# Optimization experiments

Measured on AMD Instinct MI355X. Metric: run time of the kernel, lower is better.

The kernel has to match this reference:

```python
import jax, jax.numpy as jnp
import numpy as np

B, N, DIM = 4, 8192, 1024
HEADS, DIM_HEAD = 16, 64


def setup_inputs() -> dict:
    key = jax.random.key(0)
    ks = jax.random.split(key, 6)
    s = 1.0 / np.sqrt(DIM_HEAD)
    so = 1.0 / np.sqrt(HEADS * DIM_HEAD)
    return {
        "x": jax.random.normal(ks[0], (B, N, DIM), dtype=jnp.float32),
        "Wq": jax.random.uniform(ks[1], (DIM_HEAD, DIM_HEAD), jnp.float32, -s, s),
        "Wk": jax.random.uniform(ks[2], (DIM_HEAD, DIM_HEAD), jnp.float32, -s, s),
        "Wv": jax.random.uniform(ks[3], (DIM_HEAD, DIM_HEAD), jnp.float32, -s, s),
        "Wo": jax.random.uniform(ks[4], (DIM, HEADS * DIM_HEAD), jnp.float32, -so, so),
        "bo": jax.random.uniform(ks[5], (DIM,), jnp.float32, -so, so),
    }


def reference(x, Wq, Wk, Wv, Wo, bo):
    Bs, Ns, Cs = x.shape
    # [B, H, N, Dh]
    xh = x.reshape(Bs, Ns, HEADS, DIM_HEAD).transpose(0, 2, 1, 3)
    # torch Linear: y = x @ W.T
    q = jnp.einsum('bhnd,ed->bhne', xh, Wq)
    k = jnp.einsum('bhnd,ed->bhne', xh, Wk)
    v = jnp.einsum('bhnd,ed->bhne', xh, Wv)
    # k^T v: [B, H, Dh, Dh], normalized by N (dropout is identity, p=0)
    dots = jnp.einsum('bhnd,bhne->bhde', k, v) / float(Ns)
    res = jnp.einsum('bhnd,bhde->bhne', q, dots)
    # b h n d -> b n (h d)
    res = res.transpose(0, 2, 1, 3).reshape(Bs, Ns, HEADS * DIM_HEAD)
    return res @ Wo.T + bo
```

## Files before the change

kernel.cpp:

```cpp
#include <hip/hip_runtime.h>

#define DIMC 1024
#define NSEQ 8192
#define DH 64

typedef __attribute__((ext_vector_type(8))) short short8;
typedef __attribute__((ext_vector_type(4))) float f32x4;

__device__ __forceinline__ short f2bf(float f) {
  union { float f; unsigned u; } v; v.f = f;
  unsigned r = v.u + 0x7FFFu + ((v.u >> 16) & 1u);
  return (short)(r >> 16);
}

__device__ __forceinline__ unsigned pack_bf2(float a, float b) {
  union { float f; unsigned u; } va, vb;
  va.f = a; vb.f = b;
  unsigned ua = va.u + 0x8000u;
  unsigned ub = vb.u + 0x8000u;
  return (ua >> 16) | (ub & 0xFFFF0000u);
}

__device__ __forceinline__ void gload_lds16(const void* g, void* l) {
  __builtin_amdgcn_global_load_lds(
      (const __attribute__((address_space(1))) void*)g,
      (__attribute__((address_space(3))) void*)l, 16, 0, 0);
}

__global__ __launch_bounds__(64) void gram_kernel(const float* __restrict__ x,
                                                  float* __restrict__ Gpart,
                                                  short* __restrict__ xbf) {
  int chunk = blockIdx.x, bh = blockIdx.y;
  int b = bh >> 4, h = bh & 15;
  int t = threadIdx.x;
  __shared__ __align__(16) float rows[16 * 64];
  const float* xb = x + ((size_t)b * NSEQ) * DIMC + h * DH;
  short* xo = xbf ? xbf + ((size_t)b * NSEQ) * DIMC + h * DH : (short*)0;
  int d0 = (t >> 3) * 8, e0 = (t & 7) * 8;
  float acc[8][8] = {};
  float4 v[4];
#pragma unroll
  for (int i = 0; i < 4; i++) {
    int f4 = i * 64 + t;
    v[i] = *(const float4*)(xb + (size_t)(chunk * 256 + (f4 >> 4)) * DIMC + (f4 & 15) * 4);
  }
  for (int it = 0; it < 16; it++) {
    __syncthreads();
#pragma unroll
    for (int i = 0; i < 4; i++) ((float4*)rows)[i * 64 + t] = v[i];
    __syncthreads();
    if (xo) {
#pragma unroll
      for (int i = 0; i < 4; i++) {
        int f4 = i * 64 + t;
        int row = chunk * 256 + it * 16 + (f4 >> 4), col = (f4 & 15) * 4;
        uint2 pw = {pack_bf2(v[i].x, v[i].y), pack_bf2(v[i].z, v[i].w)};
        *(uint2*)(xo + (size_t)row * DIMC + col) = pw;
      }
    }
    if (it < 15) {
      int nbase = chunk * 256 + (it + 1) * 16;
#pragma unroll
      for (int i = 0; i < 4; i++) {
        int f4 = i * 64 + t;
        v[i] = *(const float4*)(xb + (size_t)(nbase + (f4 >> 4)) * DIMC + (f4 & 15) * 4);
      }
    }
#pragma unroll
    for (int r = 0; r < 16; r++) {
      float xd[8], xe[8];
      *(float4*)&xd[0] = *(const float4*)&rows[r * 64 + d0];
      *(float4*)&xd[4] = *(const float4*)&rows[r * 64 + d0 + 4];
      *(float4*)&xe[0] = *(const float4*)&rows[r * 64 + e0];
      *(float4*)&xe[4] = *(const float4*)&rows[r * 64 + e0 + 4];
#pragma unroll
      for (int i = 0; i < 8; i++)
#pragma unroll
        for (int j = 0; j < 8; j++) acc[i][j] = fmaf(xd[i], xe[j], acc[i][j]);
    }
  }
  float* gp = Gpart + (size_t)chunk * (64 * 4096) + (size_t)bh * 4096;
#pragma unroll
  for (int i = 0; i < 8; i++)
#pragma unroll
    for (int j = 0; j < 8; j++) gp[(d0 + i) * 64 + e0 + j] = acc[i][j];
}

__global__ void reduce_g(const float* __restrict__ Gpart, float* __restrict__ G) {
  int i = blockIdx.x * 256 + threadIdx.x;
  float s = 0.f;
#pragma unroll
  for (int p = 0; p < 32; p++) s += Gpart[(size_t)p * (64 * 4096) + i];
  G[i] = s;
}

__global__ __launch_bounds__(256) void combine_kernel(
    const float* __restrict__ G, const float* __restrict__ Wq,
    const float* __restrict__ Wk, const float* __restrict__ Wv,
    const float* __restrict__ Wo, short* __restrict__ WbigT) {
  int bh = blockIdx.x, qt = blockIdx.y;
  int b = bh >> 4, h = bh & 15;
  int t = threadIdx.x;
  __shared__ __align__(16) float sG[4096];
  __shared__ __align__(16) float sW[4096];
  __shared__ __align__(16) float sA[4096];
  __shared__ __align__(16) float sM[4096];

  for (int i = t; i < 4096; i += 256) sG[i] = G[(size_t)bh * 4096 + i];
  for (int i = t; i < 4096; i += 256) sW[i] = Wk[i];
  __syncthreads();

  int d0 = (t >> 4) * 4, e0 = (t & 15) * 4;
  {
    float a[4][4] = {};
    for (int fg = 0; fg < 16; fg++) {
      float wk[4][4], g4[4][4];
#pragma unroll
      for (int i = 0; i < 4; i++) *(float4*)wk[i] = *(const float4*)&sW[(d0 + i) * 64 + fg * 4];
#pragma unroll
      for (int ff = 0; ff < 4; ff++) *(float4*)g4[ff] = *(const float4*)&sG[(fg * 4 + ff) * 64 + e0];
#pragma unroll
      for (int i = 0; i < 4; i++)
#pragma unroll
        for (int ff = 0; ff < 4; ff++)
#pragma unroll
          for (int j = 0; j < 4; j++) a[i][j] = fmaf(wk[i][ff], g4[ff][j], a[i][j]);
    }
#pragma unroll
    for (int i = 0; i < 4; i++)
#pragma unroll
      for (int j = 0; j < 4; j++) sA[(d0 + i) * 64 + e0 + j] = a[i][j];
  }
  __syncthreads();
  for (int i = t; i < 4096; i += 256) sW[i] = Wv[i];
  __syncthreads();
  {
    float a[4][4] = {};
    for (int fgi = 0; fgi < 16; fgi++) {
      int fg = (fgi + (t & 15)) & 15;
      float t1[4][4], wv[4][4];
#pragma unroll
      for (int i = 0; i < 4; i++) *(float4*)t1[i] = *(const float4*)&sA[(d0 + i) * 64 + fg * 4];
#pragma unroll
      for (int j = 0; j < 4; j++) *(float4*)wv[j] = *(const float4*)&sW[(e0 + j) * 64 + fg * 4];
#pragma unroll
      for (int i = 0; i < 4; i++)
#pragma unroll
        for (int j = 0; j < 4; j++)
#pragma unroll
          for (int ff = 0; ff < 4; ff++) a[i][j] = fmaf(t1[i][ff], wv[j][ff], a[i][j]);
    }
    __syncthreads();
#pragma unroll
    for (int i = 0; i < 4; i++)
#pragma unroll
      for (int j = 0; j < 4; j++) sG[(d0 + i) * 64 + e0 + j] = a[i][j];
  }
  __syncthreads();
  for (int i = t; i < 4096; i += 256) sW[i] = Wq[i];
  __syncthreads();
  {
    float a[4][4] = {};
    for (int f = 0; f < 64; f++) {
      float wq[4], t2[4];
      *(float4*)wq = *(const float4*)&sW[f * 64 + d0];
      *(float4*)t2 = *(const float4*)&sG[f * 64 + e0];
#pragma unroll
      for (int i = 0; i < 4; i++)
#pragma unroll
        for (int j = 0; j < 4; j++) a[i][j] = fmaf(wq[i], t2[j], a[i][j]);
    }
#pragma unroll
    for (int i = 0; i < 4; i++)
#pragma unroll
      for (int j = 0; j < 4; j++) sM[(d0 + i) * 64 + e0 + j] = a[i][j] * (1.0f / 8192.0f);
  }
  __syncthreads();
  int dd0 = (t & 15) * 4, cl0 = (t >> 4) * 4;
  for (int cc = qt * 2; cc < qt * 2 + 2; cc++) {
    int c0 = cc * 64;
    for (int i = t; i < 4096; i += 256)
      sW[i] = Wo[(size_t)(c0 + (i >> 6)) * DIMC + h * DH + (i & 63)];
    __syncthreads();
    float a[4][4] = {};
    for (int egi = 0; egi < 16; egi++) {
      int eg = (egi + (t & 15)) & 15;
      float m4[4][4], wo4[4][4];
#pragma unroll
      for (int i = 0; i < 4; i++) *(float4*)m4[i] = *(const float4*)&sM[(dd0 + i) * 64 + eg * 4];
#pragma unroll
      for (int j = 0; j < 4; j++) *(float4*)wo4[j] = *(const float4*)&sW[(cl0 + j) * 64 + eg * 4];
#pragma unroll
      for (int i = 0; i < 4; i++)
#pragma unroll
        for (int j = 0; j < 4; j++)
#pragma unroll
          for (int ff = 0; ff < 4; ff++) a[i][j] = fmaf(m4[i][ff], wo4[j][ff], a[i][j]);
    }
#pragma unroll
    for (int j = 0; j < 4; j++) {
      uint2 pw = {pack_bf2(a[0][j], a[1][j]), pack_bf2(a[2][j], a[3][j])};
      *(uint2*)&WbigT[((size_t)b << 20) + (size_t)(c0 + cl0 + j) * DIMC + h * DH + dd0] = pw;
    }
    __syncthreads();
  }
}

__global__ __launch_bounds__(256, 3) void gemm_small(
    const float* __restrict__ x, const short* __restrict__ WbigT,
    const float* __restrict__ bo, float* __restrict__ out) {
  int bid = blockIdx.x;
  int xcd = bid & 7, r = bid >> 3;
  int g = r >> 5, q = r & 31;
  int m_blk = g * 32 + xcd * 4 + (q >> 3);
  int n_blk = q & 7;
  int b = m_blk >> 6;
  int row0 = m_blk * 128;
  int c0 = n_blk * 128;

  __shared__ __align__(16) short As[128 * 32];
  __shared__ __align__(16) short Bs[128 * 32];

  int t = threadIdx.x;
  int lane = t & 63, wave = t >> 6;
  int wm = wave >> 1, wn = wave & 1;
  int quad = lane >> 4, ln = lane & 15;

  f32x4 acc[4][4];
#pragma unroll
  for (int i = 0; i < 4; i++)
#pragma unroll
    for (int j = 0; j < 4; j++) acc[i][j] = (f32x4){0.f, 0.f, 0.f, 0.f};

  const short* Bbase = WbigT + ((size_t)b << 20);

  int e_base[2], crow_[2], lc_[2];
#pragma unroll
  for (int L = 0; L < 2; L++) {
    int e = (wave * 2 + L) * 512 + lane * 8;
    e_base[L] = e;
    int crow = e >> 5;
    crow_[L] = crow;
    lc_[L] = ((e >> 3) & 3) ^ ((crow >> 1) & 3);
  }

  for (int kt = 0; kt < 32; kt++) {
    int k0 = kt * 32;
    __syncthreads();
#pragma unroll
    for (int L = 0; L < 2; L++)
      gload_lds16(Bbase + (size_t)(c0 + crow_[L]) * DIMC + k0 + lc_[L] * 8, &Bs[e_base[L]]);
#pragma unroll
    for (int qq = 0; qq < 2; qq++) {
      int elem = qq * 2048 + wave * 512 + lane * 8;
      int m = elem >> 5, kk = elem & 31;
      const float* gp = x + (size_t)(row0 + m) * DIMC + k0 + kk;
      float4 v0 = *(const float4*)gp;
      float4 v1 = *(const float4*)(gp + 4);
      unsigned w0 = pack_bf2(v0.x, v0.y), w1 = pack_bf2(v0.z, v0.w);
      unsigned w2 = pack_bf2(v1.x, v1.y), w3 = pack_bf2(v1.z, v1.w);
      unsigned tmp[4] = {w0, w1, w2, w3};
      int pe = ((elem >> 3) & 3) ^ ((m >> 1) & 3);
      *(short8*)&As[m * 32 + pe * 8] = *(short8*)tmp;
    }
    __syncthreads();
    short8 afrag[4], bfrag[4];
#pragma unroll
    for (int i = 0; i < 4; i++) {
      int ar = wm * 64 + i * 16 + ln;
      afrag[i] = *(const short8*)&As[ar * 32 + (quad ^ ((ar >> 1) & 3)) * 8];
      int br = wn * 64 + i * 16 + ln;
      bfrag[i] = *(const short8*)&Bs[br * 32 + (quad ^ ((br >> 1) & 3)) * 8];
    }
#pragma unroll
    for (int i = 0; i < 4; i++)
#pragma unroll
      for (int j = 0; j < 4; j++)
        acc[i][j] = __builtin_amdgcn_mfma_f32_16x16x32_bf16(afrag[i], bfrag[j], acc[i][j], 0, 0, 0);
  }

  float bov[4];
#pragma unroll
  for (int j = 0; j < 4; j++) bov[j] = bo[c0 + wn * 64 + j * 16 + ln];
#pragma unroll
  for (int i = 0; i < 4; i++)
#pragma unroll
    for (int j = 0; j < 4; j++) {
      int col = c0 + wn * 64 + j * 16 + ln;
#pragma unroll
      for (int rr = 0; rr < 4; rr++) {
        int row = row0 + wm * 64 + i * 16 + quad * 4 + rr;
        out[(size_t)row * DIMC + col] = acc[i][j][rr] + bov[j];
      }
    }
}

__global__ __launch_bounds__(512, 2) void gemm_big2(
    const short* __restrict__ xbf, const short* __restrict__ WbigT,
    const float* __restrict__ bo, float* __restrict__ out) {
  int bid = blockIdx.x;
  int xcd = bid & 7, r = bid >> 3;
  int m_blk = xcd * 16 + (r >> 2);
  int n_blk = r & 3;
  int b = m_blk >> 5;
  size_t row0 = (size_t)m_blk * 256;
  int c0 = n_blk * 256;

  __shared__ __align__(16) short As[2][256 * 64];
  __shared__ __align__(16) short Bs[2][256 * 64];

  int t = threadIdx.x;
  int lane = t & 63, wave = t >> 6;
  int wm = wave >> 2, wn = wave & 3;
  int quad = lane >> 4, ln = lane & 15;

  f32x4 acc[8][4];
#pragma unroll
  for (int i = 0; i < 8; i++)
#pragma unroll
    for (int j = 0; j < 4; j++) acc[i][j] = (f32x4){0.f, 0.f, 0.f, 0.f};

  const short* Bbase = WbigT + ((size_t)b << 20);

  const short* Asrc[4];
  const short* Bsrc[4];
  int doff[4];
#pragma unroll
  for (int s = 0; s < 4; s++) {
    int p = s * 512 + t;
    int row = p >> 3;
    int cl = (p & 7) ^ (row & 7);
    doff[s] = p * 8;
    Asrc[s] = xbf + (row0 + row) * (size_t)DIMC + cl * 8;
    Bsrc[s] = Bbase + (size_t)(c0 + row) * DIMC + cl * 8;
  }

  auto stage = [&](int kt, int u) {
    int k0 = kt * 64;
#pragma unroll
    for (int s = 0; s < 4; s++) gload_lds16(Asrc[s] + k0, &As[u][doff[s]]);
#pragma unroll
    for (int s = 0; s < 4; s++) gload_lds16(Bsrc[s] + k0, &Bs[u][doff[s]]);
  };

  stage(0, 0);
  stage(1, 1);

  for (int kt = 0; kt < 16; kt++) {
    if (kt < 15) asm volatile("s_waitcnt vmcnt(8)" ::: "memory");
    else         asm volatile("s_waitcnt vmcnt(0)" ::: "memory");
    __builtin_amdgcn_s_barrier();
    const short* Ab = As[kt & 1];
    const short* Bb = Bs[kt & 1];
#pragma unroll
    for (int kk = 0; kk < 2; kk++) {
      short8 af[8];
      short8 bf4[4];
#pragma unroll
      for (int i = 0; i < 8; i++) {
        int ar = wm * 128 + i * 16 + ln;
        af[i] = *(const short8*)&Ab[ar * 64 + (((kk * 4 + quad) ^ (ar & 7)) << 3)];
      }
#pragma unroll
      for (int j = 0; j < 4; j++) {
        int br = wn * 64 + j * 16 + ln;
        bf4[j] = *(const short8*)&Bb[br * 64 + (((kk * 4 + quad) ^ (br & 7)) << 3)];
      }
      __builtin_amdgcn_s_setprio(1);
#pragma unroll
      for (int i = 0; i < 8; i++)
#pragma unroll
        for (int j = 0; j < 4; j++)
          acc[i][j] = __builtin_amdgcn_mfma_f32_16x16x32_bf16(af[i], bf4[j], acc[i][j], 0, 0, 0);
      __builtin_amdgcn_s_setprio(0);
    }
    __builtin_amdgcn_s_barrier();
    asm volatile("" ::: "memory");
    if (kt < 14) stage(kt + 2, kt & 1);
  }

  float bov[4];
#pragma unroll
  for (int j = 0; j < 4; j++) bov[j] = bo[c0 + wn * 64 + j * 16 + ln];
#pragma unroll
  for (int i = 0; i < 8; i++)
#pragma unroll
    for (int j = 0; j < 4; j++) {
      int col = c0 + wn * 64 + j * 16 + ln;
#pragma unroll
      for (int rr = 0; rr < 4; rr++) {
        size_t row = row0 + wm * 128 + i * 16 + quad * 4 + rr;
        out[row * DIMC + col] = acc[i][j][rr] + bov[j];
      }
    }
}

extern "C" void kernel_launch(void* const* d_in, const int* in_sizes, int n_in,
                              void* d_out, int out_size, void* d_ws, size_t ws_size,
                              hipStream_t stream) {
  const float* x  = (const float*)d_in[0];
  const float* Wq = (const float*)d_in[1];
  const float* Wk = (const float*)d_in[2];
  const float* Wv = (const float*)d_in[3];
  const float* Wo = (const float*)d_in[4];
  const float* bo = (const float*)d_in[5];
  float* out = (float*)d_out;
  (void)in_sizes; (void)n_in; (void)out_size;

  if (ws_size >= ((size_t)105 << 20)) {
    short* xbf   = (short*)d_ws;
    float* Gpart = (float*)((char*)d_ws + ((size_t)64 << 20));
    float* G     = (float*)((char*)d_ws + ((size_t)96 << 20));
    short* WbigT = (short*)((char*)d_ws + ((size_t)97 << 20));
    gram_kernel<<<dim3(32, 64), 64, 0, stream>>>(x, Gpart, xbf);
    reduce_g<<<1024, 256, 0, stream>>>(Gpart, G);
    combine_kernel<<<dim3(64, 8), 256, 0, stream>>>(G, Wq, Wk, Wv, Wo, WbigT);
    gemm_big2<<<512, 512, 0, stream>>>(xbf, WbigT, bo, out);
  } else {
    float* Gpart = (float*)d_ws;
    float* G     = (float*)((char*)d_ws + ((size_t)32 << 20));
    short* WbigT = (short*)((char*)d_ws + ((size_t)33 << 20));
    gram_kernel<<<dim3(32, 64), 64, 0, stream>>>(x, Gpart, (short*)0);
    reduce_g<<<1024, 256, 0, stream>>>(Gpart, G);
    combine_kernel<<<dim3(64, 8), 256, 0, stream>>>(G, Wq, Wk, Wv, Wo, WbigT);
    gemm_small<<<2048, 256, 0, stream>>>(x, WbigT, bo, out);
  }
}
```

Measured before the change: 384.9 us.

## Split GEMM k-tile into four quadrant phases with barriers interleaving LDS loads and MFMA

Restructures the inner k-tile loop of the big GEMM into four sub-tile phases (A-half by B-half), each loading its fragments from LDS then issuing MFMAs, separated by workgroup barriers with priority raised during the MFMA blocks. The goal is a ping-pong schedule where waves on a SIMD alternate between LDS reads and matrix math, so LDS latency is hidden behind other waves' MFMAs. It adds six extra barriers per k-tile, and the B fragments for the first column half are read from LDS twice, which costs extra synchronization and LDS traffic.

```diff
diff --git a/kernel.cpp b/kernel.cpp
--- a/kernel.cpp
+++ b/kernel.cpp
@@ -295,7 +295,7 @@
     }
 }
 
-__global__ __launch_bounds__(512, 2) void gemm_big2(
+__global__ __launch_bounds__(512, 2) void gemm_big3(
     const short* __restrict__ xbf, const short* __restrict__ WbigT,
     const float* __restrict__ bo, float* __restrict__ out) {
   int bid = blockIdx.x;
@@ -346,38 +346,88 @@
   stage(0, 0);
   stage(1, 1);
 
+#define LD_A(dst, i, kk)                                                      \
+  {                                                                           \
+    int ar = wm * 128 + (i)*16 + ln;                                          \
+    dst = *(const short8*)&Ab[ar * 64 + ((((kk)*4 + quad) ^ (ar & 7)) << 3)]; \
+  }
+#define LD_B(dst, j, kk)                                                      \
+  {                                                                           \
+    int br = wn * 64 + (j)*16 + ln;                                           \
+    dst = *(const short8*)&Bb[br * 64 + ((((kk)*4 + quad) ^ (br & 7)) << 3)]; \
+  }
+
   for (int kt = 0; kt < 16; kt++) {
     if (kt < 15) asm volatile("s_waitcnt vmcnt(8)" ::: "memory");
     else         asm volatile("s_waitcnt vmcnt(0)" ::: "memory");
     __builtin_amdgcn_s_barrier();
     const short* Ab = As[kt & 1];
     const short* Bb = Bs[kt & 1];
-#pragma unroll
-    for (int kk = 0; kk < 2; kk++) {
-      short8 af[8];
-      short8 bf4[4];
-#pragma unroll
-      for (int i = 0; i < 8; i++) {
-        int ar = wm * 128 + i * 16 + ln;
-        af[i] = *(const short8*)&Ab[ar * 64 + (((kk * 4 + quad) ^ (ar & 7)) << 3)];
-      }
-#pragma unroll
-      for (int j = 0; j < 4; j++) {
-        int br = wn * 64 + j * 16 + ln;
-        bf4[j] = *(const short8*)&Bb[br * 64 + (((kk * 4 + quad) ^ (br & 7)) << 3)];
-      }
-      __builtin_amdgcn_s_setprio(1);
-#pragma unroll
-      for (int i = 0; i < 8; i++)
-#pragma unroll
-        for (int j = 0; j < 4; j++)
-          acc[i][j] = __builtin_amdgcn_mfma_f32_16x16x32_bf16(af[i], bf4[j], acc[i][j], 0, 0, 0);
-      __builtin_amdgcn_s_setprio(0);
-    }
+
+    short8 af0[4][2], af1[4][2], bf0[2][2], bf1[2][2], bf0b[2][2];
+#pragma unroll
+    for (int i = 0; i < 4; i++) { LD_A(af0[i][0], i, 0); LD_A(af0[i][1], i, 1); }
+#pragma unroll
+    for (int j = 0; j < 2; j++) { LD_B(bf0[j][0], j, 0); LD_B(bf0[j][1], j, 1); }
+    __builtin_amdgcn_s_barrier();
+    asm volatile("s_waitcnt lgkmcnt(0)");
+    __builtin_amdgcn_s_setprio(1);
+#pragma unroll
+    for (int i = 0; i < 4; i++)
+#pragma unroll
+      for (int j = 0; j < 2; j++)
+#pragma unroll
+        for (int kk = 0; kk < 2; kk++)
+          acc[i][j] = __builtin_amdgcn_mfma_f32_16x16x32_bf16(af0[i][kk], bf0[j][kk], acc[i][j], 0, 0, 0);
+    __builtin_amdgcn_s_setprio(0);
+    __builtin_amdgcn_s_barrier();
+#pragma unroll
+    for (int j = 0; j < 2; j++) { LD_B(bf1[j][0], j + 2, 0); LD_B(bf1[j][1], j + 2, 1); }
+    __builtin_amdgcn_s_barrier();
+    asm volatile("s_waitcnt lgkmcnt(0)");
+    __builtin_amdgcn_s_setprio(1);
+#pragma unroll
+    for (int i = 0; i < 4; i++)
+#pragma unroll
+      for (int j = 0; j < 2; j++)
+#pragma unroll
+        for (int kk = 0; kk < 2; kk++)
+          acc[i][j + 2] = __builtin_amdgcn_mfma_f32_16x16x32_bf16(af0[i][kk], bf1[j][kk], acc[i][j + 2], 0, 0, 0);
+    __builtin_amdgcn_s_setprio(0);
+    __builtin_amdgcn_s_barrier();
+#pragma unroll
+    for (int i = 0; i < 4; i++) { LD_A(af1[i][0], i + 4, 0); LD_A(af1[i][1], i + 4, 1); }
+    __builtin_amdgcn_s_barrier();
+    asm volatile("s_waitcnt lgkmcnt(0)");
+    __builtin_amdgcn_s_setprio(1);
+#pragma unroll
+    for (int i = 0; i < 4; i++)
+#pragma unroll
+      for (int j = 0; j < 2; j++)
+#pragma unroll
+        for (int kk = 0; kk < 2; kk++)
+          acc[i + 4][j + 2] = __builtin_amdgcn_mfma_f32_16x16x32_bf16(af1[i][kk], bf1[j][kk], acc[i + 4][j + 2], 0, 0, 0);
+    __builtin_amdgcn_s_setprio(0);
+    __builtin_amdgcn_s_barrier();
+#pragma unroll
+    for (int j = 0; j < 2; j++) { LD_B(bf0b[j][0], j, 0); LD_B(bf0b[j][1], j, 1); }
+    __builtin_amdgcn_s_barrier();
+    asm volatile("s_waitcnt lgkmcnt(0)");
+    __builtin_amdgcn_s_setprio(1);
+#pragma unroll
+    for (int i = 0; i < 4; i++)
+#pragma unroll
+      for (int j = 0; j < 2; j++)
+#pragma unroll
+        for (int kk = 0; kk < 2; kk++)
+          acc[i + 4][j] = __builtin_amdgcn_mfma_f32_16x16x32_bf16(af1[i][kk], bf0b[j][kk], acc[i + 4][j], 0, 0, 0);
+    __builtin_amdgcn_s_setprio(0);
     __builtin_amdgcn_s_barrier();
     asm volatile("" ::: "memory");
     if (kt < 14) stage(kt + 2, kt & 1);
   }
+#undef LD_A
+#undef LD_B
 
   float bov[4];
 #pragma unroll
@@ -415,7 +465,7 @@
     gram_kernel<<<dim3(32, 64), 64, 0, stream>>>(x, Gpart, xbf);
     reduce_g<<<1024, 256, 0, stream>>>(Gpart, G);
     combine_kernel<<<dim3(64, 8), 256, 0, stream>>>(G, Wq, Wk, Wv, Wo, WbigT);
-    gemm_big2<<<512, 512, 0, stream>>>(xbf, WbigT, bo, out);
+    gemm_big3<<<512, 512, 0, stream>>>(xbf, WbigT, bo, out);
   } else {
     float* Gpart = (float*)d_ws;
     float* G     = (float*)((char*)d_ws + ((size_t)32 << 20));
```

After: 381.1 us. About the same (-1.0%).
